# Optimization experiments

Hardware: AMD Instinct MI355X
Metric: run time of the kernel (lower is better)

Reference implementation:

```python
import jax, jax.numpy as jnp
import numpy as np

LABEL_LEN = 48
PRED_LEN = 96
D_MODEL = 512


def _pos_embed(L, d):
    pos = np.arange(L, dtype=np.float32)[:, None]
    div = np.exp(np.arange(0, d, 2, dtype=np.float32) * (-np.log(10000.0) / d))
    pe = np.zeros((L, d), np.float32)
    pe[:, 0::2] = np.sin(pos * div)
    pe[:, 1::2] = np.cos(pos * div)
    return jnp.asarray(pe)


def _embed(x, conv_w):
    # x: [B, L, C]; circular conv1d k=3 (TokenEmbedding) + sinusoidal PE
    xp = jnp.pad(jnp.transpose(x, (0, 2, 1)), ((0, 0), (0, 0), (1, 1)), mode='wrap')
    y = jax.lax.conv_general_dilated(xp, conv_w, (1,), 'VALID',
                                     dimension_numbers=('NCH', 'OIH', 'NCH'))
    y = jnp.transpose(y, (0, 2, 1))  # [B, L, D]
    return y + _pos_embed(y.shape[1], y.shape[2])


def _lstm_cell(x, h, c, Wih, Whh, b):
    g = x @ Wih.T + h @ Whh.T + b
    i, f, gg, o = jnp.split(g, 4, axis=-1)  # torch gate order i,f,g,o
    c = jax.nn.sigmoid(f) * c + jax.nn.sigmoid(i) * jnp.tanh(gg)
    h = jax.nn.sigmoid(o) * jnp.tanh(c)
    return h, c


def _lstm(xs, Wih, Whh, b):
    B, _, _ = xs.shape
    H = Whh.shape[1]
    init = (jnp.zeros((B, H), xs.dtype), jnp.zeros((B, H), xs.dtype))
    def step(carry, x):
        h, c = _lstm_cell(x, carry[0], carry[1], Wih, Whh, b)
        return (h, c), h
    (h, c), ys = jax.lax.scan(step, init, jnp.transpose(xs, (1, 0, 2)))
    return jnp.transpose(ys, (1, 0, 2)), h, c


def _forward(x_enc, x_dec, emb_enc_w, emb_dec_w, enc_Wih, enc_Whh, enc_b,
             dec_Wih, dec_Whh, dec_b, attn_W, attn_b, v, fc_W, fc_b,
             proj_W, proj_b):
    H = D_MODEL
    enc_in = _embed(x_enc, emb_enc_w)                 # [B, Le, H]
    dec_in = _embed(x_dec, emb_dec_w)                 # [B, Ld, H]
    enc_out, h0, c0 = _lstm(enc_in, enc_Wih, enc_Whh, enc_b)  # [B, Le, H]

    # precompute encoder part of Bahdanau score: attn(cat(h, enc)) splits columnwise
    Wh, We = attn_W[:, :H], attn_W[:, H:]
    enc_part = jnp.einsum('blh,kh->blk', enc_out, We) + attn_b   # [B, Le, H]
    # precompute input gates for decoded timesteps
    xs = dec_in[:, LABEL_LEN:PRED_LEN, :]                         # [B, T, H]
    xg = jnp.einsum('bth,gh->btg', xs, dec_Wih) + dec_b           # [B, T, 4H]

    def step(carry, xg_t):
        h, c = carry
        g = xg_t + h @ dec_Whh.T
        i, f, gg, o = jnp.split(g, 4, axis=-1)
        c = jax.nn.sigmoid(f) * c + jax.nn.sigmoid(i) * jnp.tanh(gg)
        h = jax.nn.sigmoid(o) * jnp.tanh(c)
        feat = jnp.tanh(enc_part + (h @ Wh.T)[:, None, :])        # [B, Le, H]
        scores = feat @ v                                          # [B, Le]
        aw = jax.nn.softmax(scores, axis=1)
        ctx = jnp.einsum('bl,blh->bh', aw, enc_out)                # [B, H]
        out = jnp.concatenate([h, ctx], axis=-1) @ fc_W.T + fc_b   # [B, H]
        return (h, c), out

    (_, _), outs = jax.lax.scan(step, (h0, c0), jnp.transpose(xg, (1, 0, 2)))
    outs = jnp.transpose(outs, (1, 0, 2))                          # [B, T, H]
    proj = outs @ proj_W.T + proj_b                                # [B, T, c_out]
    # forward slices [:, -pred_len:, :]; T = pred_len-label_len < pred_len -> identity
    return proj


def setup_inputs() -> dict:
    key = jax.random.key(0)
    ks = jax.random.split(key, 20)
    s = 0.05
    H = D_MODEL
    return {
        'x_enc': jax.random.normal(ks[0], (64, 512, 7), jnp.float32),
        'x_dec': jax.random.normal(ks[1], (64, 144, 7), jnp.float32),
        'emb_enc_w': jax.random.normal(ks[2], (H, 7, 3), jnp.float32) * s,
        'emb_dec_w': jax.random.normal(ks[3], (H, 7, 3), jnp.float32) * s,
        'enc_Wih': jax.random.normal(ks[4], (4 * H, H), jnp.float32) * s,
        'enc_Whh': jax.random.normal(ks[5], (4 * H, H), jnp.float32) * s,
        'enc_b': jax.random.normal(ks[6], (4 * H,), jnp.float32) * s,
        'dec_Wih': jax.random.normal(ks[7], (4 * H, H), jnp.float32) * s,
        'dec_Whh': jax.random.normal(ks[8], (4 * H, H), jnp.float32) * s,
        'dec_b': jax.random.normal(ks[9], (4 * H,), jnp.float32) * s,
        'attn_W': jax.random.normal(ks[10], (H, 2 * H), jnp.float32) * s,
        'attn_b': jax.random.normal(ks[11], (H,), jnp.float32) * s,
        'v': jax.random.uniform(ks[12], (H,), jnp.float32),
        'fc_W': jax.random.normal(ks[13], (H, 2 * H), jnp.float32) * s,
        'fc_b': jax.random.normal(ks[14], (H,), jnp.float32) * s,
        'proj_W': jax.random.normal(ks[15], (7, H), jnp.float32) * s,
        'proj_b': jax.random.normal(ks[16], (7,), jnp.float32) * s,
    }


def reference(x_enc, x_dec, emb_enc_w, emb_dec_w, enc_Wih, enc_Whh, enc_b,
              dec_Wih, dec_Whh, dec_b, attn_W, attn_b, v, fc_W, fc_b,
              proj_W, proj_b):
    return _forward(x_enc, x_dec, emb_enc_w, emb_dec_w, enc_Wih, enc_Whh,
                    enc_b, dec_Wih, dec_Whh, dec_b, attn_W, attn_b, v,
                    fc_W, fc_b, proj_W, proj_b)
```

## Files before the change

### kernel.cpp

```cpp
#include <hip/hip_runtime.h>
#include <hip/hip_bf16.h>


typedef short bf16x8 __attribute__((ext_vector_type(8)));
typedef float f32x4 __attribute__((ext_vector_type(4)));

static __device__ __forceinline__ float bf2f(unsigned short u){
  return __uint_as_float(((unsigned)u) << 16);
}
static __device__ __forceinline__ unsigned short f2bf(float f){
  unsigned x = __float_as_uint(f);
  return (unsigned short)((x + 0x7fffu + ((x >> 16) & 1u)) >> 16);
}
static __device__ __forceinline__ float sigm(float x){
  return __builtin_amdgcn_rcpf(1.f + __builtin_amdgcn_exp2f(-1.44269504f*x));
}
static __device__ __forceinline__ float tanh2(float x){
  return 1.f - 2.f*__builtin_amdgcn_rcpf(1.f + __builtin_amdgcn_exp2f(2.88539008f*x));
}

static __device__ __forceinline__ unsigned ldu(const unsigned* p){
  return __hip_atomic_load(p, __ATOMIC_RELAXED, __HIP_MEMORY_SCOPE_AGENT);
}
static __device__ __forceinline__ void stu(unsigned* p, unsigned v){
  __hip_atomic_store(p, v, __ATOMIC_RELAXED, __HIP_MEMORY_SCOPE_AGENT);
}
static __device__ __forceinline__ unsigned long long ldq(const unsigned long long* p){
  return __hip_atomic_load(p, __ATOMIC_RELAXED, __HIP_MEMORY_SCOPE_AGENT);
}
static __device__ __forceinline__ void stq(unsigned long long* p, unsigned long long v){
  __hip_atomic_store(p, v, __ATOMIC_RELAXED, __HIP_MEMORY_SCOPE_AGENT);
}
#define VMWAIT() __asm__ __volatile__("s_waitcnt vmcnt(0)" ::: "memory")

__global__ void cast_all_k(const float* __restrict__ a0, const float* __restrict__ a1,
                           const float* __restrict__ a2, const float* __restrict__ a3,
                           const float* __restrict__ a4, const float* __restrict__ aw,
                           unsigned short* __restrict__ d0, unsigned short* __restrict__ d1,
                           unsigned short* __restrict__ d2, unsigned short* __restrict__ d3,
                           unsigned short* __restrict__ d4,
                           unsigned short* __restrict__ wh, unsigned short* __restrict__ we){
  int i = blockIdx.x*256 + threadIdx.x;
  if (i < 1048576){ d0[i] = f2bf(a0[i]); return; }
  i -= 1048576;
  if (i < 1048576){ d1[i] = f2bf(a1[i]); return; }
  i -= 1048576;
  if (i < 1048576){ d2[i] = f2bf(a2[i]); return; }
  i -= 1048576;
  if (i < 1048576){ d3[i] = f2bf(a3[i]); return; }
  i -= 1048576;
  if (i < 524288){ d4[i] = f2bf(a4[i]); return; }
  i -= 524288;
  if (i < 262144){
    int nrow = i >> 9, k = i & 511;
    wh[i] = f2bf(aw[(size_t)nrow*1024 + k]);
    we[i] = f2bf(aw[(size_t)nrow*1024 + 512 + k]);
  }
}

__global__ __launch_bounds__(512) void embed_k(const float* __restrict__ x,
    const float* __restrict__ wconv, unsigned short* __restrict__ out,
    int Bsz, int Lx, int l0, int lcount, int mode){
  __shared__ float wl[512*21];
  __shared__ float xl[66*7];
  int nch = (lcount + 63) / 64;
  int b = blockIdx.x / nch, ci = blockIdx.x % nch;
  int tid = threadIdx.x;
  for (int i = tid; i < 512*21; i += 512) wl[i] = wconv[i];
  int lstart = l0 + ci*64;
  int cnt = l0 + lcount - lstart; if (cnt > 64) cnt = 64;
  int nwin = (cnt + 2) * 7;
  for (int i = tid; i < nwin; i += 512){
    int wr = i / 7, c = i % 7;
    int gl = lstart - 1 + wr;
    gl = (gl + Lx) % Lx;
    xl[i] = x[((size_t)b*Lx + gl)*7 + c];
  }
  __syncthreads();
  int o = tid;
  float fe = (float)(o & ~1);
  float div = __expf(fe * -0.0179889461f);
  const float* wrow = &wl[o*21];
  for (int li = 0; li < cnt; ++li){
    int l = lstart + li;
    float acc = 0.f;
    #pragma unroll
    for (int c = 0; c < 7; ++c)
      #pragma unroll
      for (int kk = 0; kk < 3; ++kk)
        acc += xl[(li + kk)*7 + c] * wrow[c*3 + kk];
    float arg = (float)l * div;
    acc += (o & 1) ? cosf(arg) : sinf(arg);
    size_t oi = mode ? (((size_t)b*lcount + (l - l0))*512 + o)
                     : (((size_t)l*Bsz + b)*512 + o);
    out[oi] = f2bf(acc);
  }
}

__global__ __launch_bounds__(256) void gemm_nt(const unsigned short* __restrict__ A, int lda,
    const unsigned short* __restrict__ Bw, int ldb, const float* __restrict__ bias,
    unsigned short* __restrict__ C, int ldc, int M, int N, int K){
  __shared__ __align__(16) unsigned short Asm[128*40];
  __shared__ __align__(16) unsigned short Bsm[128*40];
  const int tid = threadIdx.x;
  const int m0 = blockIdx.y * 128, n0 = blockIdx.x * 128;
  const int lane = tid & 63;
  const int wid = tid >> 6;
  const int wm = (wid >> 1) * 64, wn = (wid & 1) * 64;
  const int fr = lane & 15, q = lane >> 4;
  f32x4 acc[4][4];
  #pragma unroll
  for (int i=0;i<4;i++)
    #pragma unroll
    for(int j=0;j<4;j++) acc[i][j] = (f32x4){0.f,0.f,0.f,0.f};
  for (int k0 = 0; k0 < K; k0 += 32){
    #pragma unroll
    for (int c = 0; c < 2; ++c){
      int ch = tid + c*256;
      int r = ch >> 2, s = (ch & 3) * 8;
      *(uint4*)&Asm[r*40 + s] = *(const uint4*)&A[(size_t)(m0 + r)*lda + k0 + s];
      *(uint4*)&Bsm[r*40 + s] = *(const uint4*)&Bw[(size_t)(n0 + r)*ldb + k0 + s];
    }
    __syncthreads();
    bf16x8 af[4], bfv[4];
    #pragma unroll
    for (int i=0;i<4;i++){
      af[i]  = *(const bf16x8*)&Asm[(wm + i*16 + fr)*40 + q*8];
      bfv[i] = *(const bf16x8*)&Bsm[(wn + i*16 + fr)*40 + q*8];
    }
    #pragma unroll
    for (int i=0;i<4;i++)
      #pragma unroll
      for (int j=0;j<4;j++)
        acc[i][j] = __builtin_amdgcn_mfma_f32_16x16x32_bf16(af[i], bfv[j], acc[i][j], 0,0,0);
    __syncthreads();
  }
  #pragma unroll
  for (int i=0;i<4;i++){
    #pragma unroll
    for (int j=0;j<4;j++){
      int n = n0 + wn + j*16 + fr;
      float bv = bias ? bias[n] : 0.f;
      #pragma unroll
      for (int r=0;r<4;r++){
        int m = m0 + wm + i*16 + q*4 + r;
        C[(size_t)m*ldc + n] = f2bf(acc[i][j][r] + bv);
      }
    }
  }
}

__global__ __launch_bounds__(256) void gemm64_nt(const unsigned short* __restrict__ A, int lda,
    const unsigned short* __restrict__ Bw, int ldb, const float* __restrict__ bias,
    unsigned short* __restrict__ C, int ldc, int M, int N, int K){
  __shared__ __align__(16) unsigned short Asm[64*40];
  __shared__ __align__(16) unsigned short Bsm[128*40];
  const int tid = threadIdx.x;
  const int m0 = blockIdx.y * 64, n0 = blockIdx.x * 128;
  const int lane = tid & 63, wid = tid >> 6;
  const int fr = lane & 15, q = lane >> 4;
  f32x4 acc[8];
  #pragma unroll
  for (int j=0;j<8;j++) acc[j] = (f32x4){0.f,0.f,0.f,0.f};
  for (int k0 = 0; k0 < K; k0 += 32){
    {
      int r = tid >> 2, s = (tid & 3) * 8;
      *(uint4*)&Asm[r*40 + s] = *(const uint4*)&A[(size_t)(m0 + r)*lda + k0 + s];
      #pragma unroll
      for (int c = 0; c < 2; ++c){
        int ch = tid + c*256;
        int rb = ch >> 2, sb = (ch & 3) * 8;
        *(uint4*)&Bsm[rb*40 + sb] = *(const uint4*)&Bw[(size_t)(n0 + rb)*ldb + k0 + sb];
      }
    }
    __syncthreads();
    bf16x8 af = *(const bf16x8*)&Asm[(wid*16 + fr)*40 + q*8];
    #pragma unroll
    for (int j=0;j<8;j++){
      bf16x8 bv = *(const bf16x8*)&Bsm[(j*16 + fr)*40 + q*8];
      acc[j] = __builtin_amdgcn_mfma_f32_16x16x32_bf16(af, bv, acc[j], 0,0,0);
    }
    __syncthreads();
  }
  #pragma unroll
  for (int j=0;j<8;j++){
    int n = n0 + j*16 + fr;
    float bv = bias ? bias[n] : 0.f;
    #pragma unroll
    for (int r=0;r<4;r++){
      int m = m0 + wid*16 + q*4 + r;
      C[(size_t)m*ldc + n] = f2bf(acc[j][r] + bv);
    }
  }
}

__global__ __launch_bounds__(256) void gemm64_ntf(const unsigned short* __restrict__ A, int lda,
    const unsigned short* __restrict__ Bw, int ldb,
    float* __restrict__ C, int ldc, int M, int N, int K){
  __shared__ __align__(16) unsigned short Asm[64*40];
  __shared__ __align__(16) unsigned short Bsm[128*40];
  const int tid = threadIdx.x;
  const int m0 = blockIdx.y * 64, n0 = blockIdx.x * 128;
  const int lane = tid & 63, wid = tid >> 6;
  const int fr = lane & 15, q = lane >> 4;
  f32x4 acc[8];
  #pragma unroll
  for (int j=0;j<8;j++) acc[j] = (f32x4){0.f,0.f,0.f,0.f};
  for (int k0 = 0; k0 < K; k0 += 32){
    {
      int r = tid >> 2, s = (tid & 3) * 8;
      *(uint4*)&Asm[r*40 + s] = *(const uint4*)&A[(size_t)(m0 + r)*lda + k0 + s];
      #pragma unroll
      for (int c = 0; c < 2; ++c){
        int ch = tid + c*256;
        int rb = ch >> 2, sb = (ch & 3) * 8;
        *(uint4*)&Bsm[rb*40 + sb] = *(const uint4*)&Bw[(size_t)(n0 + rb)*ldb + k0 + sb];
      }
    }
    __syncthreads();
    bf16x8 af = *(const bf16x8*)&Asm[(wid*16 + fr)*40 + q*8];
    #pragma unroll
    for (int j=0;j<8;j++){
      bf16x8 bv = *(const bf16x8*)&Bsm[(j*16 + fr)*40 + q*8];
      acc[j] = __builtin_amdgcn_mfma_f32_16x16x32_bf16(af, bv, acc[j], 0,0,0);
    }
    __syncthreads();
  }
  #pragma unroll
  for (int j=0;j<8;j++){
    int n = n0 + j*16 + fr;
    #pragma unroll
    for (int r=0;r<4;r++){
      int m = m0 + wid*16 + q*4 + r;
      C[(size_t)m*ldc + n] = acc[j][r];
    }
  }
}

__global__ __launch_bounds__(512) void lstm_enc(
    const unsigned short* __restrict__ xw,
    const unsigned short* __restrict__ whh,
    float* __restrict__ cbuf, unsigned long long* __restrict__ hbuf,
    unsigned short* __restrict__ encout,
    int t0, int nsteps, unsigned* __restrict__ slots){
  __shared__ __align__(16) unsigned short wlds[128*516];
  __shared__ __align__(16) unsigned short hblds[16*516];
  __shared__ float gbufE[256*9];
  const int tid = threadIdx.x;
  const int g = blockIdx.x & 7, j = blockIdx.x >> 3;
  const int b0 = g*8, u0 = j*64;
  for (int idx = tid; idx < 128*64; idx += 512){
    int n = idx >> 6, ch = idx & 63;
    int R = (n >> 6)*512 + u0 + (n & 63);
    *(uint4*)&wlds[n*516 + ch*8] = *(const uint4*)&whh[(size_t)R*512 + ch*8];
  }
  for (int idx = tid; idx < 1032; idx += 512)
    *(unsigned long long*)&hblds[8*516 + idx*4] = 0ull;
  const int lane = tid & 63, wv = tid >> 6, fr = lane & 15, q = lane >> 4;
  const int m = tid >> 6, j2 = tid & 63;
  bf16x8 breg[16];
  {
    int rl = 128 + wv*16 + fr;
    int R2 = (rl >> 6)*512 + u0 + (rl & 63);
    const unsigned short* wp2 = &whh[(size_t)R2*512 + q*8];
    #pragma unroll
    for (int kk = 0; kk < 16; ++kk)
      breg[kk] = *(const bf16x8*)&wp2[kk*32];
  }
  float cst = cbuf[(b0 + m)*512 + u0 + j2];
  unsigned* myslot = slots + g*16 + j;
  const unsigned* gslots = slots + g*16;
  unsigned short px0, px1, px2, px3;
  {
    size_t xi = ((size_t)t0*64 + b0 + m)*2048 + u0 + j2;
    px0 = xw[xi]; px1 = xw[xi + 512]; px2 = xw[xi + 1024]; px3 = xw[xi + 1536];
  }
  __syncthreads();
  for (int s = 0; s < nsteps; ++s){
    const int t = t0 + s;
    const int rp = t & 1, wp = rp ^ 1;
    {
      const unsigned long long* hq = hbuf + (size_t)rp*8192 + (size_t)b0*128;
      unsigned long long v0 = ldq(&hq[tid]);
      unsigned long long v1 = ldq(&hq[tid + 512]);
      int b2 = tid >> 7, q2 = tid & 127;
      *(unsigned long long*)&hblds[b2*516 + q2*4] = v0;
      *(unsigned long long*)&hblds[(b2 + 4)*516 + q2*4] = v1;
    }
    __syncthreads();
    f32x4 acc = {0.f,0.f,0.f,0.f}, acc2 = {0.f,0.f,0.f,0.f};
    #pragma unroll
    for (int kk = 0; kk < 16; ++kk){
      bf16x8 av = *(const bf16x8*)&hblds[fr*516 + kk*32 + q*8];
      bf16x8 bv = *(const bf16x8*)&wlds[(wv*16 + fr)*516 + kk*32 + q*8];
      acc  = __builtin_amdgcn_mfma_f32_16x16x32_bf16(av, bv,       acc,  0,0,0);
      acc2 = __builtin_amdgcn_mfma_f32_16x16x32_bf16(av, breg[kk], acc2, 0,0,0);
    }
    if (q < 2){
      #pragma unroll
      for (int r = 0; r < 4; ++r){
        gbufE[(wv*16 + fr)*9 + q*4 + r] = acc[r];
        gbufE[(128 + wv*16 + fr)*9 + q*4 + r] = acc2[r];
      }
    }
    __syncthreads();
    unsigned short hv;
    {
      float gi = gbufE[(j2)*9 + m]        + bf2f(px0);
      float gf = gbufE[(64 + j2)*9 + m]   + bf2f(px1);
      float gg = gbufE[(128 + j2)*9 + m]  + bf2f(px2);
      float go = gbufE[(192 + j2)*9 + m]  + bf2f(px3);
      float cc = sigm(gf)*cst + sigm(gi)*tanh2(gg);
      float hh = sigm(go)*tanh2(cc);
      cst = cc;
      hv = f2bf(hh);
      unsigned other = (unsigned)__shfl_xor((int)(unsigned)hv, 1);
      unsigned pair = ((unsigned)hv) | (other << 16);
      unsigned pair2 = (unsigned)__shfl_xor((int)pair, 2);
      if ((j2 & 3) == 0){
        unsigned long long qw = (((unsigned long long)pair2) << 32) | (unsigned long long)pair;
        stq(&hbuf[(size_t)wp*8192 + (size_t)(b0+m)*128 + ((u0 + j2) >> 2)], qw);
      }
    }
    VMWAIT();
    __syncthreads();
    if (tid == 0) stu(myslot, (unsigned)(t + 1));
    encout[((size_t)(b0+m)*512 + t)*512 + u0 + j2] = hv;
    if (s == nsteps - 1) cbuf[(b0+m)*512 + u0 + j2] = cst;
    else {
      size_t xi = ((size_t)(t+1)*64 + b0 + m)*2048 + u0 + j2;
      px0 = xw[xi]; px1 = xw[xi + 512]; px2 = xw[xi + 1024]; px3 = xw[xi + 1536];
    }
    if (tid < 64){
      unsigned target = (unsigned)(t + 1);
      bool mine = (tid < 8);
      const unsigned* sp = gslots + (tid & 7);
      while (true){
        bool ok = true;
        if (mine) ok = (ldu(sp) >= target);
        if (__all(ok)) break;
        __builtin_amdgcn_s_sleep(1);
      }
    }
    __syncthreads();
  }
}

__global__ __launch_bounds__(512) void dec_h(
    const unsigned short* __restrict__ xg,
    const unsigned short* __restrict__ whh,
    const float* __restrict__ cbuf, unsigned long long* __restrict__ hbuf,
    unsigned short* __restrict__ X,
    unsigned* __restrict__ slots){
  __shared__ __align__(16) unsigned short wlds[128*516];
  __shared__ __align__(16) unsigned short hblds[16*516];
  __shared__ float gbufE[256*9];
  const int tid = threadIdx.x;
  const int g = blockIdx.x & 7, j = blockIdx.x >> 3;
  const int b0 = g*8, u0 = j*64;
  for (int idx = tid; idx < 128*64; idx += 512){
    int n = idx >> 6, ch = idx & 63;
    int R = (n >> 6)*512 + u0 + (n & 63);
    *(uint4*)&wlds[n*516 + ch*8] = *(const uint4*)&whh[(size_t)R*512 + ch*8];
  }
  for (int idx = tid; idx < 1032; idx += 512)
    *(unsigned long long*)&hblds[8*516 + idx*4] = 0ull;
  const int lane = tid & 63, wv = tid >> 6, fr = lane & 15, q = lane >> 4;
  const int m = tid >> 6, j2 = tid & 63;
  bf16x8 breg[16];
  {
    int rl = 128 + wv*16 + fr;
    int R2 = (rl >> 6)*512 + u0 + (rl & 63);
    const unsigned short* wp2 = &whh[(size_t)R2*512 + q*8];
    #pragma unroll
    for (int kk = 0; kk < 16; ++kk)
      breg[kk] = *(const bf16x8*)&wp2[kk*32];
  }
  float cst = cbuf[(b0 + m)*512 + u0 + j2];
  unsigned* myslot = slots + g*16 + j;
  const unsigned* gslots = slots + g*16;
  unsigned short px0, px1, px2, px3;
  {
    size_t xi = ((size_t)(b0 + m)*48)*2048 + u0 + j2;
    px0 = xg[xi]; px1 = xg[xi + 512]; px2 = xg[xi + 1024]; px3 = xg[xi + 1536];
  }
  __syncthreads();
  for (int t = 0; t < 48; ++t){
    const int rp = t & 1, wp = rp ^ 1;
    {
      const unsigned long long* hq = hbuf + (size_t)rp*8192 + (size_t)b0*128;
      unsigned long long v0 = ldq(&hq[tid]);
      unsigned long long v1 = ldq(&hq[tid + 512]);
      int b2 = tid >> 7, q2 = tid & 127;
      *(unsigned long long*)&hblds[b2*516 + q2*4] = v0;
      *(unsigned long long*)&hblds[(b2 + 4)*516 + q2*4] = v1;
    }
    __syncthreads();
    f32x4 acc = {0.f,0.f,0.f,0.f}, acc2 = {0.f,0.f,0.f,0.f};
    #pragma unroll
    for (int kk = 0; kk < 16; ++kk){
      bf16x8 av = *(const bf16x8*)&hblds[fr*516 + kk*32 + q*8];
      bf16x8 bv = *(const bf16x8*)&wlds[(wv*16 + fr)*516 + kk*32 + q*8];
      acc  = __builtin_amdgcn_mfma_f32_16x16x32_bf16(av, bv,       acc,  0,0,0);
      acc2 = __builtin_amdgcn_mfma_f32_16x16x32_bf16(av, breg[kk], acc2, 0,0,0);
    }
    if (q < 2){
      #pragma unroll
      for (int r = 0; r < 4; ++r){
        gbufE[(wv*16 + fr)*9 + q*4 + r] = acc[r];
        gbufE[(128 + wv*16 + fr)*9 + q*4 + r] = acc2[r];
      }
    }
    __syncthreads();
    unsigned short hv;
    {
      float gi = gbufE[(j2)*9 + m]        + bf2f(px0);
      float gf = gbufE[(64 + j2)*9 + m]   + bf2f(px1);
      float gg = gbufE[(128 + j2)*9 + m]  + bf2f(px2);
      float go = gbufE[(192 + j2)*9 + m]  + bf2f(px3);
      float cc = sigm(gf)*cst + sigm(gi)*tanh2(gg);
      float hh = sigm(go)*tanh2(cc);
      cst = cc;
      hv = f2bf(hh);
      unsigned other = (unsigned)__shfl_xor((int)(unsigned)hv, 1);
      unsigned pair = ((unsigned)hv) | (other << 16);
      unsigned pair2 = (unsigned)__shfl_xor((int)pair, 2);
      if ((j2 & 3) == 0){
        unsigned long long qw = (((unsigned long long)pair2) << 32) | (unsigned long long)pair;
        stq(&hbuf[(size_t)wp*8192 + (size_t)(b0+m)*128 + ((u0 + j2) >> 2)], qw);
      }
    }
    VMWAIT();
    __syncthreads();
    if (tid == 0) stu(myslot, (unsigned)(t + 1));
    X[((size_t)t*64 + b0 + m)*1024 + u0 + j2] = hv;
    if (t < 47){
      size_t xi = ((size_t)(b0 + m)*48 + t + 1)*2048 + u0 + j2;
      px0 = xg[xi]; px1 = xg[xi + 512]; px2 = xg[xi + 1024]; px3 = xg[xi + 1536];
    }
    if (tid < 64){
      unsigned target = (unsigned)(t + 1);
      bool mine = (tid < 8);
      const unsigned* sp = gslots + (tid & 7);
      while (true){
        bool ok = true;
        if (mine) ok = (ldu(sp) >= target);
        if (__all(ok)) break;
        __builtin_amdgcn_s_sleep(1);
      }
    }
    __syncthreads();
  }
}

__global__ __launch_bounds__(256) void attn_scores(
    const unsigned short* __restrict__ encpart,
    const float* __restrict__ hwh,
    const float* __restrict__ vvec,
    float* __restrict__ scores){
  __shared__ __align__(16) float hwhs[512];
  __shared__ __align__(16) float vm2s[512];
  __shared__ float red[4];
  const int tid = threadIdx.x;
  const int tc = blockIdx.x >> 9;
  const int b = (blockIdx.x >> 3) & 63, lc = blockIdx.x & 7;
  const int l = tid >> 2, kq = tid & 3;
  const int lane = tid & 63, wv = tid >> 6;
  vm2s[tid] = -2.f * vvec[tid];
  vm2s[tid+256] = -2.f * vvec[tid+256];
  __syncthreads();
  float vsumf;
  {
    float x = vm2s[tid] + vm2s[tid+256];
    #pragma unroll
    for (int off=32; off; off>>=1) x += __shfl_xor(x, off);
    if (lane == 0) red[wv] = x;
    __syncthreads();
    vsumf = -0.5f * (red[0]+red[1]+red[2]+red[3]);
  }
  bf16x8 epr[16];
  {
    const unsigned short* ep = encpart + ((size_t)(b*512 + lc*64 + l))*512 + kq*128;
    #pragma unroll
    for (int i = 0; i < 16; ++i) epr[i] = *(const bf16x8*)&ep[i*8];
  }
  const float C = 2.88539008f;
  for (int t = tc*12; t < tc*12 + 12; ++t){
    __syncthreads();
    hwhs[tid]     = C * hwh[((size_t)t*64 + b)*512 + tid];
    hwhs[tid+256] = C * hwh[((size_t)t*64 + b)*512 + tid + 256];
    __syncthreads();
    float sacc = 0.f;
    #pragma unroll
    for (int kk = 0; kk < 16; ++kk){
      float4 h0 = *(const float4*)&hwhs[kq*128 + kk*8];
      float4 h1 = *(const float4*)&hwhs[kq*128 + kk*8 + 4];
      float4 v0 = *(const float4*)&vm2s[kq*128 + kk*8];
      float4 v1 = *(const float4*)&vm2s[kq*128 + kk*8 + 4];
      const unsigned short* e = (const unsigned short*)&epr[kk];
      float hw[8] = {h0.x,h0.y,h0.z,h0.w,h1.x,h1.y,h1.z,h1.w};
      float vv[8] = {v0.x,v0.y,v0.z,v0.w,v1.x,v1.y,v1.z,v1.w};
      #pragma unroll
      for (int ee = 0; ee < 8; ++ee){
        float a = fmaf(bf2f(e[ee]), C, hw[ee]);
        sacc = fmaf(vv[ee], __builtin_amdgcn_rcpf(1.f + __builtin_amdgcn_exp2f(a)), sacc);
      }
    }
    sacc += __shfl_xor(sacc, 1);
    sacc += __shfl_xor(sacc, 2);
    if (kq == 0) scores[((size_t)t*64 + b)*512 + lc*64 + l] = vsumf + sacc;
  }
}

__global__ __launch_bounds__(256) void softmax_aw(
    const float* __restrict__ scores, unsigned short* __restrict__ awb){
  __shared__ float red[4];
  const int row = blockIdx.x, tid = threadIdx.x;
  const int lane = tid & 63, wv = tid >> 6;
  float v0 = scores[(size_t)row*512 + tid];
  float v1 = scores[(size_t)row*512 + tid + 256];
  float mx = fmaxf(v0, v1);
  #pragma unroll
  for (int off=32; off; off>>=1) mx = fmaxf(mx, __shfl_xor(mx, off));
  if (lane == 0) red[wv] = mx;
  __syncthreads();
  mx = fmaxf(fmaxf(red[0],red[1]), fmaxf(red[2],red[3]));
  __syncthreads();
  float e0 = __expf(v0 - mx), e1 = __expf(v1 - mx);
  float ps = e0 + e1;
  #pragma unroll
  for (int off=32; off; off>>=1) ps += __shfl_xor(ps, off);
  if (lane == 0) red[wv] = ps;
  __syncthreads();
  float inv = 1.f / (red[0]+red[1]+red[2]+red[3]);
  awb[(size_t)row*512 + tid]       = f2bf(e0 * inv);
  awb[(size_t)row*512 + tid + 256] = f2bf(e1 * inv);
}

__global__ __launch_bounds__(256) void ctx_k(
    const unsigned short* __restrict__ awb,
    const unsigned short* __restrict__ encout,
    unsigned short* __restrict__ X){
  __shared__ unsigned short awt[512*12];
  const int tid = threadIdx.x;
  const int b = blockIdx.x >> 2, t0 = (blockIdx.x & 3)*12;
  for (int i = tid; i < 12*256; i += 256){
    int tt = i >> 8, d = i & 255;
    unsigned u = *(const unsigned*)&awb[((size_t)(t0+tt)*64 + b)*512 + d*2];
    awt[(2*d)*12 + tt]   = (unsigned short)(u & 0xffffu);
    awt[(2*d+1)*12 + tt] = (unsigned short)(u >> 16);
  }
  __syncthreads();
  float a0[12], a1[12];
  #pragma unroll
  for (int j = 0; j < 12; ++j){ a0[j] = 0.f; a1[j] = 0.f; }
  const unsigned* eo = (const unsigned*)(encout + (size_t)b*512*512) + tid;
  for (int ll = 0; ll < 512; ++ll){
    unsigned ee = eo[(size_t)ll*256];
    float e0 = __uint_as_float((ee & 0xffffu) << 16);
    float e1 = __uint_as_float(ee & 0xffff0000u);
    const unsigned* wp2 = (const unsigned*)&awt[ll*12];
    float w[12];
    #pragma unroll
    for (int z = 0; z < 6; ++z){
      unsigned wu = wp2[z];
      w[2*z]   = bf2f((unsigned short)(wu & 0xffffu));
      w[2*z+1] = bf2f((unsigned short)(wu >> 16));
    }
    #pragma unroll
    for (int j = 0; j < 12; ++j){
      a0[j] = fmaf(w[j], e0, a0[j]);
      a1[j] = fmaf(w[j], e1, a1[j]);
    }
  }
  #pragma unroll
  for (int j = 0; j < 12; ++j){
    size_t r = (size_t)(t0+j)*64 + b;
    unsigned pk = ((unsigned)f2bf(a0[j])) | (((unsigned)f2bf(a1[j])) << 16);
    *(unsigned*)&X[r*1024 + 512 + 2*tid] = pk;
  }
}

__global__ void proj_k(const unsigned short* __restrict__ outs,
                       const float* __restrict__ pw, const float* __restrict__ pb,
                       float* __restrict__ out){
  int gid = blockIdx.x*256 + threadIdx.x;
  if (gid >= 64*48*7) return;
  int r = gid / 7, oc = gid % 7;
  int b = r & 63, t = r >> 6;
  const unsigned short* orow = outs + (size_t)r*512;
  const float* wrow = pw + oc*512;
  float s = pb[oc];
  for (int k = 0; k < 512; k += 8){
    bf16x8 o8 = *(const bf16x8*)&orow[k];
    #pragma unroll
    for (int e=0;e<8;e++) s += bf2f(((unsigned short*)&o8)[e]) * wrow[k+e];
  }
  out[((size_t)b*48 + t)*7 + oc] = s;
}

extern "C" void kernel_launch(void* const* d_in, const int* in_sizes, int n_in,
                              void* d_out, int out_size, void* d_ws, size_t ws_size,
                              hipStream_t stream){
  (void)in_sizes; (void)n_in; (void)out_size; (void)ws_size;
  const float* x_enc   = (const float*)d_in[0];
  const float* x_dec   = (const float*)d_in[1];
  const float* w_emb_e = (const float*)d_in[2];
  const float* w_emb_d = (const float*)d_in[3];
  const float* enc_Wih = (const float*)d_in[4];
  const float* enc_Whh = (const float*)d_in[5];
  const float* enc_b   = (const float*)d_in[6];
  const float* dec_Wih = (const float*)d_in[7];
  const float* dec_Whh = (const float*)d_in[8];
  const float* dec_b   = (const float*)d_in[9];
  const float* attn_W  = (const float*)d_in[10];
  const float* attn_b  = (const float*)d_in[11];
  const float* vvec    = (const float*)d_in[12];
  const float* fc_W    = (const float*)d_in[13];
  const float* fc_b    = (const float*)d_in[14];
  const float* proj_W  = (const float*)d_in[15];
  const float* proj_b  = (const float*)d_in[16];
  float* out = (float*)d_out;

  char* ws = (char*)d_ws;
  size_t off = 0;
  auto alloc = [&](size_t bytes)->char*{
    char* p = ws + off;
    off = (off + bytes + 255) & ~(size_t)255;
    return p;
  };
  unsigned short* encxw  = (unsigned short*)alloc(512ull*64*2048*2);
  unsigned short* encin  = (unsigned short*)alloc(512ull*64*512*2);
  unsigned short* encout = (unsigned short*)alloc(64ull*512*512*2);
  unsigned short* xs     = (unsigned short*)alloc(64ull*48*512*2);
  unsigned short* xg     = (unsigned short*)alloc(64ull*48*2048*2);
  unsigned short* Xb     = (unsigned short*)alloc(3072ull*1024*2);
  float* hwh    = (float*)alloc(3072ull*512*4);
  float* scores = (float*)alloc(3072ull*512*4);
  unsigned short* awb    = (unsigned short*)alloc(3072ull*512*2);
  unsigned short* outsb  = (unsigned short*)alloc(3072ull*512*2);
  unsigned short* wih_e  = (unsigned short*)alloc(2048ull*512*2);
  unsigned short* whh_e  = (unsigned short*)alloc(2048ull*512*2);
  unsigned short* wih_d  = (unsigned short*)alloc(2048ull*512*2);
  unsigned short* whh_d  = (unsigned short*)alloc(2048ull*512*2);
  unsigned short* whq    = (unsigned short*)alloc(512ull*512*2);
  unsigned short* weq    = (unsigned short*)alloc(512ull*512*2);
  unsigned short* fcw    = (unsigned short*)alloc(512ull*1024*2);
  unsigned long long* hbuf = (unsigned long long*)alloc(2ull*64*128*8);
  float* cbuf   = (float*)alloc(64ull*512*4);
  unsigned* eslots = (unsigned*)alloc(4*64*4);
  unsigned* dslots = (unsigned*)alloc(4*64*4);

  hipMemsetAsync(hbuf, 0, 2ull*64*128*8, stream);
  hipMemsetAsync(cbuf, 0, 64ull*512*4, stream);
  hipMemsetAsync(eslots, 0, 4*64*4, stream);
  hipMemsetAsync(dslots, 0, 4*64*4, stream);

  cast_all_k<<<19456, 256, 0, stream>>>(enc_Wih, enc_Whh, dec_Wih, dec_Whh, fc_W, attn_W,
                                        wih_e, whh_e, wih_d, whh_d, fcw, whq, weq);

  embed_k<<<512, 512, 0, stream>>>(x_enc, w_emb_e, encin, 64, 512, 0, 512, 0);
  embed_k<<<64, 512, 0, stream>>>(x_dec, w_emb_d, xs, 64, 144, 48, 48, 1);

  gemm64_nt<<<dim3(16, 48), 256, 0, stream>>>(xs, 512, wih_d, 512, dec_b, xg, 2048, 3072, 2048, 512);

  gemm_nt<<<dim3(16, 256), 256, 0, stream>>>(encin, 512, wih_e, 512, enc_b, encxw, 2048, 32768, 2048, 512);
  lstm_enc<<<64, 512, 0, stream>>>(encxw, whh_e, cbuf, hbuf, encout, 0, 512, eslots);

  gemm_nt<<<dim3(4, 256), 256, 0, stream>>>(encout, 512, weq, 512, attn_b, encin, 512, 32768, 512, 512);

  dec_h<<<64, 512, 0, stream>>>(xg, whh_d, cbuf, hbuf, Xb, dslots);

  gemm64_ntf<<<dim3(4, 48), 256, 0, stream>>>(Xb, 1024, whq, 512, hwh, 512, 3072, 512, 512);

  attn_scores<<<2048, 256, 0, stream>>>(encin , hwh, vvec, scores);
  softmax_aw<<<3072, 256, 0, stream>>>(scores, awb);
  ctx_k<<<256, 256, 0, stream>>>(awb, encout, Xb);

  gemm64_nt<<<dim3(4, 48), 256, 0, stream>>>(Xb, 1024, fcw, 1024, fc_b, outsb, 512, 3072, 512, 1024);

  proj_k<<<84, 256, 0, stream>>>(outsb, proj_W, proj_b, out);
}
```

Measured before the change: 2.249 ms.

## Merge prep kernels, pair input-gate GEMMs, and fuse softmax into context kernel

Merges the weight casts and both embedding launches into one prep kernel. The encoder and decoder input-gate GEMMs now run in a single launch that splits work by block index. Softmax is folded into the context kernel, so the bf16 attention-weight buffer and its kernel are gone. The aim is to cut launch overhead and the round trip of attention weights through global memory. In exchange, ctx_k now runs 12 serial softmaxes per block with extra barriers, and 512-thread cast blocks carry unused shared memory.

```diff
diff --git a/kernel.cpp b/kernel.cpp
--- a/kernel.cpp
+++ b/kernel.cpp
@@ -33,14 +33,61 @@
 }
 #define VMWAIT() __asm__ __volatile__("s_waitcnt vmcnt(0)" ::: "memory")
 
-__global__ void cast_all_k(const float* __restrict__ a0, const float* __restrict__ a1,
-                           const float* __restrict__ a2, const float* __restrict__ a3,
-                           const float* __restrict__ a4, const float* __restrict__ aw,
-                           unsigned short* __restrict__ d0, unsigned short* __restrict__ d1,
-                           unsigned short* __restrict__ d2, unsigned short* __restrict__ d3,
-                           unsigned short* __restrict__ d4,
-                           unsigned short* __restrict__ wh, unsigned short* __restrict__ we){
-  int i = blockIdx.x*256 + threadIdx.x;
+__global__ __launch_bounds__(512) void prep_k(
+    const float* __restrict__ x_enc, const float* __restrict__ x_dec,
+    const float* __restrict__ w_emb_e, const float* __restrict__ w_emb_d,
+    unsigned short* __restrict__ encin, unsigned short* __restrict__ xs,
+    const float* __restrict__ a0, const float* __restrict__ a1,
+    const float* __restrict__ a2, const float* __restrict__ a3,
+    const float* __restrict__ a4, const float* __restrict__ aw,
+    unsigned short* __restrict__ d0, unsigned short* __restrict__ d1,
+    unsigned short* __restrict__ d2, unsigned short* __restrict__ d3,
+    unsigned short* __restrict__ d4,
+    unsigned short* __restrict__ wh, unsigned short* __restrict__ we){
+  __shared__ float wl[512*21];
+  __shared__ float xl[66*7];
+  const int bid = blockIdx.x, tid = threadIdx.x;
+  if (bid < 576){
+    const float* x; const float* wconv; unsigned short* outp;
+    int Lx, l0, lcount, mode, nch, rel;
+    if (bid < 512){ x = x_enc; wconv = w_emb_e; outp = encin;
+                    Lx = 512; l0 = 0; lcount = 512; mode = 0; nch = 8; rel = bid; }
+    else          { x = x_dec; wconv = w_emb_d; outp = xs;
+                    Lx = 144; l0 = 48; lcount = 48; mode = 1; nch = 1; rel = bid - 512; }
+    const int Bsz = 64;
+    int b = rel / nch, ci = rel % nch;
+    for (int i = tid; i < 512*21; i += 512) wl[i] = wconv[i];
+    int lstart = l0 + ci*64;
+    int cnt = l0 + lcount - lstart; if (cnt > 64) cnt = 64;
+    int nwin = (cnt + 2) * 7;
+    for (int i = tid; i < nwin; i += 512){
+      int wr = i / 7, c = i % 7;
+      int gl = lstart - 1 + wr;
+      gl = (gl + Lx) % Lx;
+      xl[i] = x[((size_t)b*Lx + gl)*7 + c];
+    }
+    __syncthreads();
+    int o = tid;
+    float fe = (float)(o & ~1);
+    float div = __expf(fe * -0.0179889461f);
+    const float* wrow = &wl[o*21];
+    for (int li = 0; li < cnt; ++li){
+      int l = lstart + li;
+      float acc = 0.f;
+      #pragma unroll
+      for (int c = 0; c < 7; ++c)
+        #pragma unroll
+        for (int kk = 0; kk < 3; ++kk)
+          acc += xl[(li + kk)*7 + c] * wrow[c*3 + kk];
+      float arg = (float)l * div;
+      acc += (o & 1) ? cosf(arg) : sinf(arg);
+      size_t oi = mode ? (((size_t)b*lcount + (l - l0))*512 + o)
+                       : (((size_t)l*Bsz + b)*512 + o);
+      outp[oi] = f2bf(acc);
+    }
+    return;
+  }
+  int i = (bid - 576)*512 + tid;
   if (i < 1048576){ d0[i] = f2bf(a0[i]); return; }
   i -= 1048576;
   if (i < 1048576){ d1[i] = f2bf(a1[i]); return; }
@@ -58,45 +105,6 @@
   }
 }
 
-__global__ __launch_bounds__(512) void embed_k(const float* __restrict__ x,
-    const float* __restrict__ wconv, unsigned short* __restrict__ out,
-    int Bsz, int Lx, int l0, int lcount, int mode){
-  __shared__ float wl[512*21];
-  __shared__ float xl[66*7];
-  int nch = (lcount + 63) / 64;
-  int b = blockIdx.x / nch, ci = blockIdx.x % nch;
-  int tid = threadIdx.x;
-  for (int i = tid; i < 512*21; i += 512) wl[i] = wconv[i];
-  int lstart = l0 + ci*64;
-  int cnt = l0 + lcount - lstart; if (cnt > 64) cnt = 64;
-  int nwin = (cnt + 2) * 7;
-  for (int i = tid; i < nwin; i += 512){
-    int wr = i / 7, c = i % 7;
-    int gl = lstart - 1 + wr;
-    gl = (gl + Lx) % Lx;
-    xl[i] = x[((size_t)b*Lx + gl)*7 + c];
-  }
-  __syncthreads();
-  int o = tid;
-  float fe = (float)(o & ~1);
-  float div = __expf(fe * -0.0179889461f);
-  const float* wrow = &wl[o*21];
-  for (int li = 0; li < cnt; ++li){
-    int l = lstart + li;
-    float acc = 0.f;
-    #pragma unroll
-    for (int c = 0; c < 7; ++c)
-      #pragma unroll
-      for (int kk = 0; kk < 3; ++kk)
-        acc += xl[(li + kk)*7 + c] * wrow[c*3 + kk];
-    float arg = (float)l * div;
-    acc += (o & 1) ? cosf(arg) : sinf(arg);
-    size_t oi = mode ? (((size_t)b*lcount + (l - l0))*512 + o)
-                     : (((size_t)l*Bsz + b)*512 + o);
-    out[oi] = f2bf(acc);
-  }
-}
-
 __global__ __launch_bounds__(256) void gemm_nt(const unsigned short* __restrict__ A, int lda,
     const unsigned short* __restrict__ Bw, int ldb, const float* __restrict__ bias,
     unsigned short* __restrict__ C, int ldc, int M, int N, int K){
@@ -145,6 +153,102 @@
       for (int r=0;r<4;r++){
         int m = m0 + wm + i*16 + q*4 + r;
         C[(size_t)m*ldc + n] = f2bf(acc[i][j][r] + bv);
+      }
+    }
+  }
+}
+
+__global__ __launch_bounds__(256) void gemm_pair_k(
+    const unsigned short* __restrict__ A1, const unsigned short* __restrict__ B1,
+    const float* __restrict__ bias1, unsigned short* __restrict__ C1,
+    const unsigned short* __restrict__ A2, const unsigned short* __restrict__ B2,
+    const float* __restrict__ bias2, unsigned short* __restrict__ C2){
+  __shared__ __align__(16) unsigned short Asm[128*40];
+  __shared__ __align__(16) unsigned short Bsm[128*40];
+  const int tid = threadIdx.x;
+  const int lane = tid & 63;
+  const int fr = lane & 15, q = lane >> 4;
+  if ((int)blockIdx.x < 4096){
+    const int bx = blockIdx.x & 15, by = blockIdx.x >> 4;
+    const int m0 = by * 128, n0 = bx * 128;
+    const int wid = tid >> 6;
+    const int wm = (wid >> 1) * 64, wn = (wid & 1) * 64;
+    f32x4 acc[4][4];
+    #pragma unroll
+    for (int i=0;i<4;i++)
+      #pragma unroll
+      for(int j=0;j<4;j++) acc[i][j] = (f32x4){0.f,0.f,0.f,0.f};
+    for (int k0 = 0; k0 < 512; k0 += 32){
+      #pragma unroll
+      for (int c = 0; c < 2; ++c){
+        int ch = tid + c*256;
+        int r = ch >> 2, s = (ch & 3) * 8;
+        *(uint4*)&Asm[r*40 + s] = *(const uint4*)&A1[(size_t)(m0 + r)*512 + k0 + s];
+        *(uint4*)&Bsm[r*40 + s] = *(const uint4*)&B1[(size_t)(n0 + r)*512 + k0 + s];
+      }
+      __syncthreads();
+      bf16x8 af[4], bfv[4];
+      #pragma unroll
+      for (int i=0;i<4;i++){
+        af[i]  = *(const bf16x8*)&Asm[(wm + i*16 + fr)*40 + q*8];
+        bfv[i] = *(const bf16x8*)&Bsm[(wn + i*16 + fr)*40 + q*8];
+      }
+      #pragma unroll
+      for (int i=0;i<4;i++)
+        #pragma unroll
+        for (int j=0;j<4;j++)
+          acc[i][j] = __builtin_amdgcn_mfma_f32_16x16x32_bf16(af[i], bfv[j], acc[i][j], 0,0,0);
+      __syncthreads();
+    }
+    #pragma unroll
+    for (int i=0;i<4;i++){
+      #pragma unroll
+      for (int j=0;j<4;j++){
+        int n = n0 + wn + j*16 + fr;
+        float bv = bias1[n];
+        #pragma unroll
+        for (int r=0;r<4;r++){
+          int m = m0 + wm + i*16 + q*4 + r;
+          C1[(size_t)m*2048 + n] = f2bf(acc[i][j][r] + bv);
+        }
+      }
+    }
+  } else {
+    const int b2 = blockIdx.x - 4096;
+    const int bx = b2 & 15, by = b2 >> 4;
+    const int m0 = by * 64, n0 = bx * 128;
+    const int wid = tid >> 6;
+    f32x4 acc[8];
+    #pragma unroll
+    for (int j=0;j<8;j++) acc[j] = (f32x4){0.f,0.f,0.f,0.f};
+    for (int k0 = 0; k0 < 512; k0 += 32){
+      {
+        int r = tid >> 2, s = (tid & 3) * 8;
+        *(uint4*)&Asm[r*40 + s] = *(const uint4*)&A2[(size_t)(m0 + r)*512 + k0 + s];
+        #pragma unroll
+        for (int c = 0; c < 2; ++c){
+          int ch = tid + c*256;
+          int rb = ch >> 2, sb = (ch & 3) * 8;
+          *(uint4*)&Bsm[rb*40 + sb] = *(const uint4*)&B2[(size_t)(n0 + rb)*512 + k0 + sb];
+        }
+      }
+      __syncthreads();
+      bf16x8 af = *(const bf16x8*)&Asm[(wid*16 + fr)*40 + q*8];
+      #pragma unroll
+      for (int j=0;j<8;j++){
+        bf16x8 bv = *(const bf16x8*)&Bsm[(j*16 + fr)*40 + q*8];
+        acc[j] = __builtin_amdgcn_mfma_f32_16x16x32_bf16(af, bv, acc[j], 0,0,0);
+      }
+      __syncthreads();
+    }
+    #pragma unroll
+    for (int j=0;j<8;j++){
+      int n = n0 + j*16 + fr;
+      float bv = bias2[n];
+      #pragma unroll
+      for (int r=0;r<4;r++){
+        int m = m0 + wid*16 + q*4 + r;
+        C2[(size_t)m*2048 + n] = f2bf(acc[j][r] + bv);
       }
     }
   }
@@ -512,45 +616,37 @@
   }
 }
 
-__global__ __launch_bounds__(256) void softmax_aw(
-    const float* __restrict__ scores, unsigned short* __restrict__ awb){
-  __shared__ float red[4];
-  const int row = blockIdx.x, tid = threadIdx.x;
-  const int lane = tid & 63, wv = tid >> 6;
-  float v0 = scores[(size_t)row*512 + tid];
-  float v1 = scores[(size_t)row*512 + tid + 256];
-  float mx = fmaxf(v0, v1);
-  #pragma unroll
-  for (int off=32; off; off>>=1) mx = fmaxf(mx, __shfl_xor(mx, off));
-  if (lane == 0) red[wv] = mx;
-  __syncthreads();
-  mx = fmaxf(fmaxf(red[0],red[1]), fmaxf(red[2],red[3]));
-  __syncthreads();
-  float e0 = __expf(v0 - mx), e1 = __expf(v1 - mx);
-  float ps = e0 + e1;
-  #pragma unroll
-  for (int off=32; off; off>>=1) ps += __shfl_xor(ps, off);
-  if (lane == 0) red[wv] = ps;
-  __syncthreads();
-  float inv = 1.f / (red[0]+red[1]+red[2]+red[3]);
-  awb[(size_t)row*512 + tid]       = f2bf(e0 * inv);
-  awb[(size_t)row*512 + tid + 256] = f2bf(e1 * inv);
-}
-
 __global__ __launch_bounds__(256) void ctx_k(
-    const unsigned short* __restrict__ awb,
+    const float* __restrict__ scores,
     const unsigned short* __restrict__ encout,
     unsigned short* __restrict__ X){
   __shared__ unsigned short awt[512*12];
+  __shared__ float red[4];
   const int tid = threadIdx.x;
   const int b = blockIdx.x >> 2, t0 = (blockIdx.x & 3)*12;
-  for (int i = tid; i < 12*256; i += 256){
-    int tt = i >> 8, d = i & 255;
-    unsigned u = *(const unsigned*)&awb[((size_t)(t0+tt)*64 + b)*512 + d*2];
-    awt[(2*d)*12 + tt]   = (unsigned short)(u & 0xffffu);
-    awt[(2*d+1)*12 + tt] = (unsigned short)(u >> 16);
-  }
-  __syncthreads();
+  const int lane = tid & 63, wv = tid >> 6;
+  for (int tt = 0; tt < 12; ++tt){
+    size_t row = (size_t)(t0 + tt)*64 + b;
+    float v0 = scores[row*512 + tid];
+    float v1 = scores[row*512 + tid + 256];
+    float mx = fmaxf(v0, v1);
+    #pragma unroll
+    for (int off=32; off; off>>=1) mx = fmaxf(mx, __shfl_xor(mx, off));
+    if (lane == 0) red[wv] = mx;
+    __syncthreads();
+    mx = fmaxf(fmaxf(red[0],red[1]), fmaxf(red[2],red[3]));
+    __syncthreads();
+    float e0 = __expf(v0 - mx), e1 = __expf(v1 - mx);
+    float ps = e0 + e1;
+    #pragma unroll
+    for (int off=32; off; off>>=1) ps += __shfl_xor(ps, off);
+    if (lane == 0) red[wv] = ps;
+    __syncthreads();
+    float inv = 1.f / (red[0]+red[1]+red[2]+red[3]);
+    awt[tid*12 + tt]        = f2bf(e0 * inv);
+    awt[(tid + 256)*12 + tt] = f2bf(e1 * inv);
+    __syncthreads();
+  }
   float a0[12], a1[12];
   #pragma unroll
   for (int j = 0; j < 12; ++j){ a0[j] = 0.f; a1[j] = 0.f; }
@@ -637,7 +733,6 @@
   unsigned short* Xb     = (unsigned short*)alloc(3072ull*1024*2);
   float* hwh    = (float*)alloc(3072ull*512*4);
   float* scores = (float*)alloc(3072ull*512*4);
-  unsigned short* awb    = (unsigned short*)alloc(3072ull*512*2);
   unsigned short* outsb  = (unsigned short*)alloc(3072ull*512*2);
   unsigned short* wih_e  = (unsigned short*)alloc(2048ull*512*2);
   unsigned short* whh_e  = (unsigned short*)alloc(2048ull*512*2);
@@ -656,15 +751,13 @@
   hipMemsetAsync(eslots, 0, 4*64*4, stream);
   hipMemsetAsync(dslots, 0, 4*64*4, stream);
 
-  cast_all_k<<<19456, 256, 0, stream>>>(enc_Wih, enc_Whh, dec_Wih, dec_Whh, fc_W, attn_W,
-                                        wih_e, whh_e, wih_d, whh_d, fcw, whq, weq);
-
-  embed_k<<<512, 512, 0, stream>>>(x_enc, w_emb_e, encin, 64, 512, 0, 512, 0);
-  embed_k<<<64, 512, 0, stream>>>(x_dec, w_emb_d, xs, 64, 144, 48, 48, 1);
-
-  gemm64_nt<<<dim3(16, 48), 256, 0, stream>>>(xs, 512, wih_d, 512, dec_b, xg, 2048, 3072, 2048, 512);
-
-  gemm_nt<<<dim3(16, 256), 256, 0, stream>>>(encin, 512, wih_e, 512, enc_b, encxw, 2048, 32768, 2048, 512);
+  prep_k<<<10304, 512, 0, stream>>>(x_enc, x_dec, w_emb_e, w_emb_d, encin, xs,
+                                    enc_Wih, enc_Whh, dec_Wih, dec_Whh, fc_W, attn_W,
+                                    wih_e, whh_e, wih_d, whh_d, fcw, whq, weq);
+
+  gemm_pair_k<<<4864, 256, 0, stream>>>(encin, wih_e, enc_b, encxw,
+                                        xs, wih_d, dec_b, xg);
+
   lstm_enc<<<64, 512, 0, stream>>>(encxw, whh_e, cbuf, hbuf, encout, 0, 512, eslots);
 
   gemm_nt<<<dim3(4, 256), 256, 0, stream>>>(encout, 512, weq, 512, attn_b, encin, 512, 32768, 512, 512);
@@ -674,8 +767,7 @@
   gemm64_ntf<<<dim3(4, 48), 256, 0, stream>>>(Xb, 1024, whq, 512, hwh, 512, 3072, 512, 512);
 
   attn_scores<<<2048, 256, 0, stream>>>(encin , hwh, vvec, scores);
-  softmax_aw<<<3072, 256, 0, stream>>>(scores, awb);
-  ctx_k<<<256, 256, 0, stream>>>(awb, encout, Xb);
+  ctx_k<<<256, 256, 0, stream>>>(scores, encout, Xb);
 
   gemm64_nt<<<dim3(4, 48), 256, 0, stream>>>(Xb, 1024, fcw, 1024, fc_b, outsb, 512, 3072, 512, 1024);
 
```

Result: no change. 2.217 ms (median of 2 runs) (-1.4%).
